# Performance work log

Measured on AMD Instinct MI355X. Metric: run time of the kernel, lower is better.

Reference implementation:

```python
import jax, jax.numpy as jnp
import numpy as np

N = 65536          # nodes
E = 1_048_576      # edges (avg degree 16)
IN_DIM = 16        # input_irreps = 16x0e
OUT_DIM = 8        # output_irreps = 8x0e
S_MUL = 32         # hidden 0e multiplicity
V_MUL = 16         # hidden 1o multiplicity
HID = S_MUL + 3 * V_MUL  # 80
LAYERS = 3
DEG = 16.0


def fctp(feat, eattr, w1, w2, w3, w4):
    """FullyConnectedTensorProduct(hidden x '1x0e+1x1o' -> hidden) per edge.
    Paths: 0e*0e->0e, 1o*1o->0e (dot, CG 1/sqrt(3)), 0e*1o->1o, 1o*0e->1o.
    Path weights mix multiplicities; e3nn-style fan-in normalization."""
    s1 = feat[:, :S_MUL]                         # [E, 32]
    v1 = feat[:, S_MUL:].reshape(-1, V_MUL, 3)   # [E, 16, 3]
    s2 = eattr[:, 0]                             # [E]
    v2 = eattr[:, 1:4]                           # [E, 3]
    c = 1.0 / np.sqrt(2.0)  # two paths per output irrep
    out_s = c * (jnp.einsum('ea,e,ac->ec', s1, s2, w1) / np.sqrt(S_MUL)
                 + jnp.einsum('eak,ek,ac->ec', v1, v2, w2) / np.sqrt(3.0 * V_MUL))
    out_v = c * (jnp.einsum('ea,ek,ac->eck', s1, v2, w3) / np.sqrt(S_MUL)
                 + jnp.einsum('eak,e,ac->eck', v1, s2, w4) / np.sqrt(V_MUL))
    return jnp.concatenate([out_s, out_v.reshape(-1, 3 * V_MUL)], axis=-1)


def setup_inputs() -> dict:
    key = jax.random.key(0)
    ks = jax.random.split(key, 12)
    inp = {
        'x': jax.random.normal(ks[0], (N, IN_DIM), jnp.float32),
        'edge_index': jax.random.randint(ks[1], (2, E), 0, N, jnp.int64 if jax.config.jax_enable_x64 else jnp.int32),
        'edge_attr': jax.random.normal(ks[2], (E, 4), jnp.float32),
        'W_in': jax.random.normal(ks[3], (IN_DIM, HID), jnp.float32) / np.sqrt(IN_DIM),
        'b_in': jnp.zeros((HID,), jnp.float32),
        'tp_w1': jax.random.normal(ks[4], (LAYERS, S_MUL, S_MUL), jnp.float32),
        'tp_w2': jax.random.normal(ks[5], (LAYERS, V_MUL, S_MUL), jnp.float32),
        'tp_w3': jax.random.normal(ks[6], (LAYERS, S_MUL, V_MUL), jnp.float32),
        'tp_w4': jax.random.normal(ks[7], (LAYERS, V_MUL, V_MUL), jnp.float32),
        'W_out': jax.random.normal(ks[8], (HID, OUT_DIM), jnp.float32) / np.sqrt(HID),
        'b_out': jnp.zeros((OUT_DIM,), jnp.float32),
    }
    return inp


def reference(x, edge_index, edge_attr, W_in, b_in, tp_w1, tp_w2, tp_w3, tp_w4, W_out, b_out):
    src, dst = edge_index[0], edge_index[1]
    h = x @ W_in + b_in                                   # [N, 80]
    for l in range(LAYERS):
        m = fctp(h[src], edge_attr, tp_w1[l], tp_w2[l], tp_w3[l], tp_w4[l])  # [E, 80]
        h = jax.ops.segment_sum(m, dst, num_segments=N) / np.sqrt(DEG)       # [N, 80]
    h = jax.nn.relu(h)
    return h @ W_out + b_out                              # [N, 8]
```

## Files before the change

kernel.cpp:

```cpp
#include <hip/hip_runtime.h>

#define NN 65536
#define NE 1048576
#define HID 80
#define CAP 8192

typedef unsigned int u32;
typedef unsigned short u16;
typedef unsigned long long u64;

typedef float v4f __attribute__((ext_vector_type(4)));

__device__ __forceinline__ u16 f2bf(float f) {
  u32 u = __float_as_uint(f);
  u = (u + 0x7fffu + ((u >> 16) & 1u)) >> 16;
  return (u16)u;
}
__device__ __forceinline__ float bfhi(u32 packed) {
  return __uint_as_float(packed & 0xffff0000u);
}
__device__ __forceinline__ float bflo(u32 packed) {
  return __uint_as_float(packed << 16);
}
__device__ __forceinline__ float4 ntload4f(const float4* p) {
  v4f v = __builtin_nontemporal_load((const v4f*)p);
  return make_float4(v.x, v.y, v.z, v.w);
}
__device__ __forceinline__ int ntloadi(const int* p) {
  return __builtin_nontemporal_load(p);
}

__global__ __launch_bounds__(256) void k_p1_in(const int* __restrict__ dst,
    const int* __restrict__ src, const float4* __restrict__ eattr,
    int* __restrict__ bcnt, uint4* __restrict__ tmp,
    const float* __restrict__ x, const float* __restrict__ W,
    const float* __restrict__ b, u16* __restrict__ hmain,
    u16* __restrict__ htail) {
  if (blockIdx.x < 512) {
    __shared__ int hist[256];
    __shared__ int lofs[257];
    __shared__ int gbase[256];
    __shared__ int sc[256];
    __shared__ uint4 buf[2048];
    int t = threadIdx.x;
    hist[t] = 0;
    __syncthreads();
    uint4 rec[8];
    int bk[8], lr[8];
    int base = blockIdx.x * 2048 + t;
#pragma unroll
    for (int k = 0; k < 8; k++) {
      int idx = base + k * 256;
      int d = ntloadi(dst + idx);
      float4 ea = ntload4f(eattr + idx);
      int s = ntloadi(src + idx);
      u32 c01 = (u32)f2bf(ea.x) | ((u32)f2bf(ea.y) << 16);
      u32 c23 = (u32)f2bf(ea.z) | ((u32)f2bf(ea.w) << 16);
      rec[k] = make_uint4((u32)s, c01, c23, (u32)d);
      bk[k] = d >> 8;
      lr[k] = atomicAdd(&hist[bk[k]], 1);
    }
    __syncthreads();
    int h = hist[t];
    gbase[t] = atomicAdd(&bcnt[t], h);
    sc[t] = h;
    __syncthreads();
    for (int d = 1; d < 256; d <<= 1) {
      int v = (t >= d) ? sc[t - d] : 0;
      __syncthreads();
      sc[t] += v;
      __syncthreads();
    }
    lofs[t] = sc[t] - h;
    if (t == 255) lofs[256] = 2048;
    __syncthreads();
#pragma unroll
    for (int k = 0; k < 8; k++) buf[lofs[bk[k]] + lr[k]] = rec[k];
    __syncthreads();
#pragma unroll
    for (int k = 0; k < 8; k++) {
      int j = t + k * 256;
      int lo = 0, hi = 256;
      while (hi - lo > 1) {
        int mid = (lo + hi) >> 1;
        if (lofs[mid] <= j) lo = mid;
        else hi = mid;
      }
      tmp[(size_t)lo * CAP + gbase[lo] + (j - lofs[lo])] = buf[j];
    }
  } else {
    int idx = (blockIdx.x - 512) * 256 + threadIdx.x;
    if (idx >= NN * 10) return;
    int n = idx / 10, part = idx % 10;
    const float4* xr = (const float4*)(x + (size_t)n * 16);
    float4 x0 = xr[0], x1 = xr[1], x2 = xr[2], x3 = xr[3];
    const float xs[16] = {x0.x, x0.y, x0.z, x0.w, x1.x, x1.y, x1.z, x1.w,
                          x2.x, x2.y, x2.z, x2.w, x3.x, x3.y, x3.z, x3.w};
    float acc[8];
#pragma unroll
    for (int j = 0; j < 8; j++) acc[j] = b[part * 8 + j];
#pragma unroll
    for (int k = 0; k < 16; k++) {
#pragma unroll
      for (int j = 0; j < 8; j++) acc[j] += xs[k] * W[k * HID + part * 8 + j];
    }
    u32 p0 = (u32)f2bf(acc[0]) | ((u32)f2bf(acc[1]) << 16);
    u32 p1 = (u32)f2bf(acc[2]) | ((u32)f2bf(acc[3]) << 16);
    u32 p2 = (u32)f2bf(acc[4]) | ((u32)f2bf(acc[5]) << 16);
    u32 p3 = (u32)f2bf(acc[6]) | ((u32)f2bf(acc[7]) << 16);
    uint4 vv = make_uint4(p0, p1, p2, p3);
    if (part < 8)
      *(uint4*)(hmain + (size_t)n * 64 + part * 8) = vv;
    else
      *(uint4*)(htail + (size_t)n * 16 + (part - 8) * 8) = vv;
  }
}

__global__ __launch_bounds__(256) void k_p15(const int* __restrict__ bcnt,
    const uint4* __restrict__ tmp, int* __restrict__ counts_tot,
    int* __restrict__ offsets, int* __restrict__ bucketsum) {
  __shared__ int hist[256];
  __shared__ int sc[256];
  int t = threadIdx.x;
  int b = blockIdx.x;
  hist[t] = 0;
  __syncthreads();
  int cnt = bcnt[b];
  const int* tw = (const int*)(tmp + (size_t)b * CAP);
  for (int j = t; j < cnt; j += 256) atomicAdd(&hist[tw[j * 4 + 3] & 255], 1);
  __syncthreads();
  int deg = hist[t];
  int p = (deg + 7) & ~7;
  sc[t] = p;
  __syncthreads();
  for (int d = 1; d < 256; d <<= 1) {
    int v = (t >= d) ? sc[t - d] : 0;
    __syncthreads();
    sc[t] += v;
    __syncthreads();
  }
  counts_tot[b * 256 + t] = deg;
  offsets[b * 256 + t] = sc[t] - p;
  if (t == 255) bucketsum[b] = sc[255];
}

__global__ __launch_bounds__(256) void k_p2(const int* __restrict__ bcnt,
    const uint4* __restrict__ tmp, const int* __restrict__ offsets,
    const int* __restrict__ bucketsum, const int* __restrict__ counts_tot,
    uint4* __restrict__ erec, int* __restrict__ offs_fin,
    int* __restrict__ brank, int* __restrict__ bidx, int* __restrict__ dcnt) {
  int t = threadIdx.x;
  if (blockIdx.x < 256) {
    __shared__ int bsum[256];
    __shared__ int cur[256];
    __shared__ int noff[256];
    if (t < 64) {
      int v0 = bucketsum[t * 4], v1 = bucketsum[t * 4 + 1];
      int v2 = bucketsum[t * 4 + 2], v3 = bucketsum[t * 4 + 3];
      int s = v0 + v1 + v2 + v3;
      int incl = s;
#pragma unroll
      for (int d = 1; d < 64; d <<= 1) {
        int o = __shfl_up(incl, d, 64);
        if (t >= d) incl += o;
      }
      int base = incl - s;
      bsum[t * 4] = base;
      bsum[t * 4 + 1] = base + v0;
      bsum[t * 4 + 2] = base + v0 + v1;
      bsum[t * 4 + 3] = base + v0 + v1 + v2;
    }
    cur[t] = 0;
    __syncthreads();
    int b = blockIdx.x;
    int off = offsets[b * 256 + t] + bsum[b];
    noff[t] = off;
    offs_fin[b * 256 + t] = off;
    __syncthreads();
    int cnt = bcnt[b];
    const uint4* tb = tmp + (size_t)b * CAP;
    for (int j = t; j < cnt; j += 256) {
      uint4 r = tb[j];
      int i = r.w & 255;
      int lr = atomicAdd(&cur[i], 1);
      erec[noff[i] + lr] = make_uint4(r.x, r.y, r.z, 0u);
    }
    __syncthreads();
    int deg = cur[t];
    int degp = (deg + 7) & ~7;
    uint4 z = make_uint4(0u, 0u, 0u, 0u);
    for (int e = deg; e < degp; e++) erec[noff[t] + e] = z;
  } else {
    int n = (blockIdx.x - 256) * 256 + t;
    int degp = (counts_tot[n] + 7) & ~7;
    int bb2 = 15 - min(degp >> 3, 15);
    int lane = t & 63;
    int base = 0;
#pragma unroll 1
    for (int bb = 0; bb < 16; bb++) {
      u64 m = __ballot(bb2 == bb);
      if (bb2 == bb) {
        int leader = __ffsll((long long)m) - 1;
        int lr = __popcll(m & ((lane == 63) ? ~0ull >> 1 : ((1ull << lane) - 1)));
        int bs = 0;
        if (lane == leader) bs = atomicAdd(&dcnt[bb], __popcll(m));
        bs = __shfl(bs, leader, 64);
        base = bs + lr;
      }
    }
    brank[n] = base;
    bidx[n] = bb2;
  }
}

__global__ __launch_bounds__(256) void k_p3(const int* __restrict__ dcnt,
    const int* __restrict__ brank, const int* __restrict__ bidx,
    int* __restrict__ nperm) {
  __shared__ int dsum[16];
  int t = threadIdx.x;
  if (t < 16) {
    int v = dcnt[t];
    int incl = v;
#pragma unroll
    for (int d = 1; d < 16; d <<= 1) {
      int o = __shfl_up(incl, d, 64);
      if (t >= d) incl += o;
    }
    dsum[t] = incl - v;
  }
  __syncthreads();
  int n = blockIdx.x * 256 + t;
  nperm[dsum[bidx[n]] + brank[n]] = n;
}

template <int LAST>
__global__ __launch_bounds__(128, 3) void k_msg(const u16* __restrict__ hmain,
    const u16* __restrict__ htail, u16* __restrict__ omain,
    u16* __restrict__ otail,
    const float* __restrict__ w1, const float* __restrict__ w2,
    const float* __restrict__ w3, const float* __restrict__ w4,
    const int* __restrict__ offsets, const int* __restrict__ counts,
    const int* __restrict__ nperm, const uint4* __restrict__ erec,
    const float* __restrict__ Wout, const float* __restrict__ bout,
    float* __restrict__ outp) {
  __shared__ float Rlds[8][4][81];
  int tid = threadIdx.x;
  const int q = tid >> 4;
  const int c = tid & 15;
  const int n = nperm[blockIdx.x * 8 + q];

  float R[4][5];
#pragma unroll
  for (int j = 0; j < 4; j++)
#pragma unroll
    for (int i = 0; i < 5; i++) R[j][i] = 0.f;

  const int start = offsets[n];
  const int degp = (counts[n] + 7) & ~7;
  const int B = degp >> 3;
  const uint2* hrow = (const uint2*)hmain + c;
  const u16* trow = htail + c;

  int i = 0;
  for (; i + 2 <= B; i += 2) {
    const int baseA = start + 8 * i;
    const int baseB = baseA + 8;
    uint4 rA[8], rB[8];
#pragma unroll
    for (int k = 0; k < 8; k++) rA[k] = erec[baseA + k];
#pragma unroll
    for (int k = 0; k < 8; k++) rB[k] = erec[baseB + k];
    uint2 hA[8], hB[8];
    u32 tA[8], tB[8];
#pragma unroll
    for (int k = 0; k < 8; k++) {
      size_t s16 = (size_t)rA[k].x * 16;
      hA[k] = hrow[s16];
      tA[k] = trow[s16];
    }
#pragma unroll
    for (int k = 0; k < 8; k++) {
      size_t s16 = (size_t)rB[k].x * 16;
      hB[k] = hrow[s16];
      tB[k] = trow[s16];
    }
#pragma unroll
    for (int k = 0; k < 8; k++) {
      float A0 = bflo(hA[k].x), A1 = bfhi(hA[k].x);
      float A2 = bflo(hA[k].y), A3 = bfhi(hA[k].y);
      float A4 = bflo(tA[k]);
      float f0 = bflo(rA[k].y), f1 = bfhi(rA[k].y);
      float f2 = bflo(rA[k].z), f3 = bfhi(rA[k].z);
      R[0][0] += f0 * A0; R[0][1] += f0 * A1; R[0][2] += f0 * A2;
      R[0][3] += f0 * A3; R[0][4] += f0 * A4;
      R[1][0] += f1 * A0; R[1][1] += f1 * A1; R[1][2] += f1 * A2;
      R[1][3] += f1 * A3; R[1][4] += f1 * A4;
      R[2][0] += f2 * A0; R[2][1] += f2 * A1; R[2][2] += f2 * A2;
      R[2][3] += f2 * A3; R[2][4] += f2 * A4;
      R[3][0] += f3 * A0; R[3][1] += f3 * A1; R[3][2] += f3 * A2;
      R[3][3] += f3 * A3; R[3][4] += f3 * A4;
    }
#pragma unroll
    for (int k = 0; k < 8; k++) {
      float A0 = bflo(hB[k].x), A1 = bfhi(hB[k].x);
      float A2 = bflo(hB[k].y), A3 = bfhi(hB[k].y);
      float A4 = bflo(tB[k]);
      float f0 = bflo(rB[k].y), f1 = bfhi(rB[k].y);
      float f2 = bflo(rB[k].z), f3 = bfhi(rB[k].z);
      R[0][0] += f0 * A0; R[0][1] += f0 * A1; R[0][2] += f0 * A2;
      R[0][3] += f0 * A3; R[0][4] += f0 * A4;
      R[1][0] += f1 * A0; R[1][1] += f1 * A1; R[1][2] += f1 * A2;
      R[1][3] += f1 * A3; R[1][4] += f1 * A4;
      R[2][0] += f2 * A0; R[2][1] += f2 * A1; R[2][2] += f2 * A2;
      R[2][3] += f2 * A3; R[2][4] += f2 * A4;
      R[3][0] += f3 * A0; R[3][1] += f3 * A1; R[3][2] += f3 * A2;
      R[3][3] += f3 * A3; R[3][4] += f3 * A4;
    }
  }
  if (i < B) {
    const int baseA = start + 8 * i;
    uint4 rA[8];
#pragma unroll
    for (int k = 0; k < 8; k++) rA[k] = erec[baseA + k];
    uint2 hA[8];
    u32 tA[8];
#pragma unroll
    for (int k = 0; k < 8; k++) {
      size_t s16 = (size_t)rA[k].x * 16;
      hA[k] = hrow[s16];
      tA[k] = trow[s16];
    }
#pragma unroll
    for (int k = 0; k < 8; k++) {
      float A0 = bflo(hA[k].x), A1 = bfhi(hA[k].x);
      float A2 = bflo(hA[k].y), A3 = bfhi(hA[k].y);
      float A4 = bflo(tA[k]);
      float f0 = bflo(rA[k].y), f1 = bfhi(rA[k].y);
      float f2 = bflo(rA[k].z), f3 = bfhi(rA[k].z);
      R[0][0] += f0 * A0; R[0][1] += f0 * A1; R[0][2] += f0 * A2;
      R[0][3] += f0 * A3; R[0][4] += f0 * A4;
      R[1][0] += f1 * A0; R[1][1] += f1 * A1; R[1][2] += f1 * A2;
      R[1][3] += f1 * A3; R[1][4] += f1 * A4;
      R[2][0] += f2 * A0; R[2][1] += f2 * A1; R[2][2] += f2 * A2;
      R[2][3] += f2 * A3; R[2][4] += f2 * A4;
      R[3][0] += f3 * A0; R[3][1] += f3 * A1; R[3][2] += f3 * A2;
      R[3][3] += f3 * A3; R[3][4] += f3 * A4;
    }
  }

#pragma unroll
  for (int j = 0; j < 4; j++) {
#pragma unroll
    for (int k = 0; k < 4; k++) Rlds[q][j][4 * c + k] = R[j][k];
    Rlds[q][j][64 + c] = R[j][4];
  }

  const float C1 = 0.03125f;
  const float C2 = 0.025515518f;
  const float C3 = 0.03125f;
  const float C4 = 0.044194174f;

  u16* opm = omain + (size_t)n * 64;

  float s0 = 0.f, s1 = 0.f;
#pragma unroll
  for (int a = 0; a < 32; a++) {
    float rs = Rlds[q][0][a];
    s0 += rs * w1[a * 32 + c];
    s1 += rs * w1[a * 32 + c + 16];
  }
  float t0 = 0.f, t1 = 0.f;
#pragma unroll
  for (int a = 0; a < 16; a++) {
    float T = Rlds[q][1][32 + 3 * a] + Rlds[q][2][33 + 3 * a] +
              Rlds[q][3][34 + 3 * a];
    t0 += T * w2[a * 32 + c];
    t1 += T * w2[a * 32 + c + 16];
  }

  float y[8];
  if (LAST) {
#pragma unroll
    for (int j = 0; j < 8; j++) y[j] = 0.f;
    float vs0 = C1 * s0 + C2 * t0;
    float vs1 = C1 * s1 + C2 * t1;
    vs0 = vs0 > 0.f ? vs0 : 0.f;
    vs1 = vs1 > 0.f ? vs1 : 0.f;
#pragma unroll
    for (int j = 0; j < 8; j++)
      y[j] += vs0 * Wout[c * 8 + j] + vs1 * Wout[(c + 16) * 8 + j];
  } else {
    opm[c] = f2bf(C1 * s0 + C2 * t0);
    opm[c + 16] = f2bf(C1 * s1 + C2 * t1);
  }

#pragma unroll
  for (int v2 = 0; v2 < 3; v2++) {
    int c2 = 32 + 16 * v2 + c;
    int cv = (c2 - 32) / 3, k = (c2 - 32) % 3;
    float a3 = 0.f, a4 = 0.f;
#pragma unroll
    for (int a = 0; a < 32; a++) a3 += Rlds[q][k + 1][a] * w3[a * 16 + cv];
#pragma unroll
    for (int a = 0; a < 16; a++)
      a4 += Rlds[q][0][32 + 3 * a + k] * w4[a * 16 + cv];
    float val = C3 * a3 + C4 * a4;
    if (LAST) {
      val = val > 0.f ? val : 0.f;
#pragma unroll
      for (int j = 0; j < 8; j++) y[j] += val * Wout[c2 * 8 + j];
    } else {
      u16 v = f2bf(val);
      if (v2 < 2) opm[32 + 16 * v2 + c] = v;
      else otail[(size_t)n * 16 + c] = v;
    }
  }

  if (LAST) {
#pragma unroll
    for (int m = 1; m <= 8; m <<= 1) {
#pragma unroll
      for (int j = 0; j < 8; j++) y[j] += __shfl_xor(y[j], m, 64);
    }
    float w = y[0];
#pragma unroll
    for (int j = 1; j < 8; j++)
      if (c == j) w = y[j];
    if (c < 8) outp[(size_t)n * 8 + c] = w + bout[c];
  }
}

extern "C" void kernel_launch(void* const* d_in, const int* in_sizes, int n_in,
                              void* d_out, int out_size, void* d_ws,
                              size_t ws_size, hipStream_t stream) {
  const float* x = (const float*)d_in[0];
  const int* ei = (const int*)d_in[1];
  const float* eattr = (const float*)d_in[2];
  const float* W_in = (const float*)d_in[3];
  const float* b_in = (const float*)d_in[4];
  const float* tp_w1 = (const float*)d_in[5];
  const float* tp_w2 = (const float*)d_in[6];
  const float* tp_w3 = (const float*)d_in[7];
  const float* tp_w4 = (const float*)d_in[8];
  const float* W_out = (const float*)d_in[9];
  const float* b_out = (const float*)d_in[10];
  float* out = (float*)d_out;

  char* ws = (char*)d_ws;
  size_t off = 0;
  auto alloc = [&](size_t bytes) {
    void* p = ws + off;
    off += (bytes + 255) & ~size_t(255);
    return p;
  };
  const size_t NEP = (size_t)NE + 8 * (size_t)NN;
  u16* hm_a = (u16*)alloc((size_t)NN * 64 * 2);
  u16* ht_a = (u16*)alloc((size_t)NN * 16 * 2);
  u16* hm_b = (u16*)alloc((size_t)NN * 64 * 2);
  u16* ht_b = (u16*)alloc((size_t)NN * 16 * 2);
  int* bcnt = (int*)alloc(256 * 4);
  int* dcnt = (int*)alloc(16 * 4);
  int* counts_tot = (int*)alloc((size_t)NN * 4);
  int* offsets = (int*)alloc((size_t)NN * 4);
  int* offs_fin = (int*)alloc((size_t)NN * 4);
  int* bucketsum = (int*)alloc(256 * 4);
  int* brank = (int*)alloc((size_t)NN * 4);
  int* bidx = (int*)alloc((size_t)NN * 4);
  int* nperm = (int*)alloc((size_t)NN * 4);
  uint4* tmp = (uint4*)alloc((size_t)256 * CAP * 16);
  uint4* erec = (uint4*)alloc(NEP * 16);

  const int* src = ei;
  const int* dst = ei + NE;

  hipMemsetAsync(bcnt, 0, 1024 + 256, stream);
  k_p1_in<<<512 + (NN * 10 + 255) / 256, 256, 0, stream>>>(
      dst, src, (const float4*)eattr, bcnt, tmp, x, W_in, b_in, hm_a, ht_a);
  k_p15<<<256, 256, 0, stream>>>(bcnt, tmp, counts_tot, offsets, bucketsum);
  k_p2<<<512, 256, 0, stream>>>(bcnt, tmp, offsets, bucketsum, counts_tot,
                                erec, offs_fin, brank, bidx, dcnt);
  k_p3<<<256, 256, 0, stream>>>(dcnt, brank, bidx, nperm);

  u16* hmi = hm_a;
  u16* hti = ht_a;
  u16* hmo = hm_b;
  u16* hto = ht_b;
  for (int l = 0; l < 2; l++) {
    k_msg<0><<<NN / 8, 128, 0, stream>>>(hmi, hti, hmo, hto, tp_w1 + l * 1024,
                                         tp_w2 + l * 512, tp_w3 + l * 512,
                                         tp_w4 + l * 256, offs_fin, counts_tot,
                                         nperm, erec, W_out, b_out, out);
    u16* t;
    t = hmi; hmi = hmo; hmo = t;
    t = hti; hti = hto; hto = t;
  }
  k_msg<1><<<NN / 8, 128, 0, stream>>>(hmi, hti, hmo, hto, tp_w1 + 2048,
                                       tp_w2 + 1024, tp_w3 + 1024, tp_w4 + 512,
                                       offs_fin, counts_tot, nperm, erec,
                                       W_out, b_out, out);
}
```

Baseline: 344.1 us.

## Merge bucket histogram and scatter kernels using fixed per-bucket edge capacity

Fuses the per-bucket degree histogram kernel and the scatter kernel into one 512-thread kernel. Each coarse bucket now gets a fixed ECAP-sized region of the edge record array, which removes the global bucket-sum prefix scan and the intermediate offsets and bucketsum buffers. The first partition pass also uses twice as many blocks with half the edges each. This drops one launch and one global round trip, at the cost of a larger padded edge array and a bucket overflow risk if a bucket's padded degree total exceeds ECAP.

```diff
diff --git a/kernel.cpp b/kernel.cpp
--- a/kernel.cpp
+++ b/kernel.cpp
@@ -3,7 +3,8 @@
 #define NN 65536
 #define NE 1048576
 #define HID 80
-#define CAP 8192
+#define TCAP 8192
+#define ECAP 8192
 
 typedef unsigned int u32;
 typedef unsigned short u16;
@@ -36,20 +37,20 @@
     const float* __restrict__ x, const float* __restrict__ W,
     const float* __restrict__ b, u16* __restrict__ hmain,
     u16* __restrict__ htail) {
-  if (blockIdx.x < 512) {
+  if (blockIdx.x < 1024) {
     __shared__ int hist[256];
     __shared__ int lofs[257];
     __shared__ int gbase[256];
     __shared__ int sc[256];
-    __shared__ uint4 buf[2048];
+    __shared__ uint4 buf[1024];
     int t = threadIdx.x;
     hist[t] = 0;
     __syncthreads();
-    uint4 rec[8];
-    int bk[8], lr[8];
-    int base = blockIdx.x * 2048 + t;
-#pragma unroll
-    for (int k = 0; k < 8; k++) {
+    uint4 rec[4];
+    int bk[4], lr[4];
+    int base = blockIdx.x * 1024 + t;
+#pragma unroll
+    for (int k = 0; k < 4; k++) {
       int idx = base + k * 256;
       int d = ntloadi(dst + idx);
       float4 ea = ntload4f(eattr + idx);
@@ -72,13 +73,13 @@
       __syncthreads();
     }
     lofs[t] = sc[t] - h;
-    if (t == 255) lofs[256] = 2048;
-    __syncthreads();
-#pragma unroll
-    for (int k = 0; k < 8; k++) buf[lofs[bk[k]] + lr[k]] = rec[k];
-    __syncthreads();
-#pragma unroll
-    for (int k = 0; k < 8; k++) {
+    if (t == 255) lofs[256] = 1024;
+    __syncthreads();
+#pragma unroll
+    for (int k = 0; k < 4; k++) buf[lofs[bk[k]] + lr[k]] = rec[k];
+    __syncthreads();
+#pragma unroll
+    for (int k = 0; k < 4; k++) {
       int j = t + k * 256;
       int lo = 0, hi = 256;
       while (hi - lo > 1) {
@@ -86,10 +87,10 @@
         if (lofs[mid] <= j) lo = mid;
         else hi = mid;
       }
-      tmp[(size_t)lo * CAP + gbase[lo] + (j - lofs[lo])] = buf[j];
+      tmp[(size_t)lo * TCAP + gbase[lo] + (j - lofs[lo])] = buf[j];
     }
   } else {
-    int idx = (blockIdx.x - 512) * 256 + threadIdx.x;
+    int idx = (blockIdx.x - 1024) * 256 + threadIdx.x;
     if (idx >= NN * 10) return;
     int n = idx / 10, part = idx % 10;
     const float4* xr = (const float4*)(x + (size_t)n * 16);
@@ -116,83 +117,58 @@
   }
 }
 
-__global__ __launch_bounds__(256) void k_p15(const int* __restrict__ bcnt,
+__global__ __launch_bounds__(512) void k_p2m(const int* __restrict__ bcnt,
     const uint4* __restrict__ tmp, int* __restrict__ counts_tot,
-    int* __restrict__ offsets, int* __restrict__ bucketsum) {
+    int* __restrict__ offs_fin, uint4* __restrict__ erec,
+    int* __restrict__ brank, int* __restrict__ bidx, int* __restrict__ dcnt) {
   __shared__ int hist[256];
   __shared__ int sc[256];
+  __shared__ int noff[256];
+  __shared__ int cur[256];
   int t = threadIdx.x;
+  if (t < 256) {
+    hist[t] = 0;
+    cur[t] = 0;
+  }
+  __syncthreads();
   int b = blockIdx.x;
-  hist[t] = 0;
-  __syncthreads();
   int cnt = bcnt[b];
-  const int* tw = (const int*)(tmp + (size_t)b * CAP);
-  for (int j = t; j < cnt; j += 256) atomicAdd(&hist[tw[j * 4 + 3] & 255], 1);
-  __syncthreads();
-  int deg = hist[t];
-  int p = (deg + 7) & ~7;
-  sc[t] = p;
+  const uint4* tb = tmp + (size_t)b * TCAP;
+  const int* tw = (const int*)tb;
+  for (int j = t; j < cnt; j += 512) atomicAdd(&hist[tw[j * 4 + 3] & 255], 1);
+  __syncthreads();
+  int deg = 0, p = 0;
+  if (t < 256) {
+    deg = hist[t];
+    p = (deg + 7) & ~7;
+    sc[t] = p;
+  }
   __syncthreads();
   for (int d = 1; d < 256; d <<= 1) {
-    int v = (t >= d) ? sc[t - d] : 0;
-    __syncthreads();
-    sc[t] += v;
-    __syncthreads();
-  }
-  counts_tot[b * 256 + t] = deg;
-  offsets[b * 256 + t] = sc[t] - p;
-  if (t == 255) bucketsum[b] = sc[255];
-}
-
-__global__ __launch_bounds__(256) void k_p2(const int* __restrict__ bcnt,
-    const uint4* __restrict__ tmp, const int* __restrict__ offsets,
-    const int* __restrict__ bucketsum, const int* __restrict__ counts_tot,
-    uint4* __restrict__ erec, int* __restrict__ offs_fin,
-    int* __restrict__ brank, int* __restrict__ bidx, int* __restrict__ dcnt) {
-  int t = threadIdx.x;
-  if (blockIdx.x < 256) {
-    __shared__ int bsum[256];
-    __shared__ int cur[256];
-    __shared__ int noff[256];
-    if (t < 64) {
-      int v0 = bucketsum[t * 4], v1 = bucketsum[t * 4 + 1];
-      int v2 = bucketsum[t * 4 + 2], v3 = bucketsum[t * 4 + 3];
-      int s = v0 + v1 + v2 + v3;
-      int incl = s;
-#pragma unroll
-      for (int d = 1; d < 64; d <<= 1) {
-        int o = __shfl_up(incl, d, 64);
-        if (t >= d) incl += o;
-      }
-      int base = incl - s;
-      bsum[t * 4] = base;
-      bsum[t * 4 + 1] = base + v0;
-      bsum[t * 4 + 2] = base + v0 + v1;
-      bsum[t * 4 + 3] = base + v0 + v1 + v2;
-    }
-    cur[t] = 0;
-    __syncthreads();
-    int b = blockIdx.x;
-    int off = offsets[b * 256 + t] + bsum[b];
+    int v = (t < 256 && t >= d) ? sc[t - d] : 0;
+    __syncthreads();
+    if (t < 256) sc[t] += v;
+    __syncthreads();
+  }
+  if (t < 256) {
+    int off = b * ECAP + sc[t] - p;
     noff[t] = off;
     offs_fin[b * 256 + t] = off;
-    __syncthreads();
-    int cnt = bcnt[b];
-    const uint4* tb = tmp + (size_t)b * CAP;
-    for (int j = t; j < cnt; j += 256) {
-      uint4 r = tb[j];
-      int i = r.w & 255;
-      int lr = atomicAdd(&cur[i], 1);
-      erec[noff[i] + lr] = make_uint4(r.x, r.y, r.z, 0u);
-    }
-    __syncthreads();
-    int deg = cur[t];
+    counts_tot[b * 256 + t] = deg;
+  }
+  __syncthreads();
+  for (int j = t; j < cnt; j += 512) {
+    uint4 r = tb[j];
+    int i = r.w & 255;
+    int lr = atomicAdd(&cur[i], 1);
+    erec[(size_t)noff[i] + lr] = make_uint4(r.x, r.y, r.z, 0u);
+  }
+  __syncthreads();
+  if (t < 256) {
     int degp = (deg + 7) & ~7;
     uint4 z = make_uint4(0u, 0u, 0u, 0u);
-    for (int e = deg; e < degp; e++) erec[noff[t] + e] = z;
-  } else {
-    int n = (blockIdx.x - 256) * 256 + t;
-    int degp = (counts_tot[n] + 7) & ~7;
+    for (int e = deg; e < degp; e++) erec[(size_t)noff[t] + e] = z;
+    int n = b * 256 + t;
     int bb2 = 15 - min(degp >> 3, 15);
     int lane = t & 63;
     int base = 0;
@@ -453,7 +429,6 @@
     off += (bytes + 255) & ~size_t(255);
     return p;
   };
-  const size_t NEP = (size_t)NE + 8 * (size_t)NN;
   u16* hm_a = (u16*)alloc((size_t)NN * 64 * 2);
   u16* ht_a = (u16*)alloc((size_t)NN * 16 * 2);
   u16* hm_b = (u16*)alloc((size_t)NN * 64 * 2);
@@ -461,24 +436,21 @@
   int* bcnt = (int*)alloc(256 * 4);
   int* dcnt = (int*)alloc(16 * 4);
   int* counts_tot = (int*)alloc((size_t)NN * 4);
-  int* offsets = (int*)alloc((size_t)NN * 4);
   int* offs_fin = (int*)alloc((size_t)NN * 4);
-  int* bucketsum = (int*)alloc(256 * 4);
   int* brank = (int*)alloc((size_t)NN * 4);
   int* bidx = (int*)alloc((size_t)NN * 4);
   int* nperm = (int*)alloc((size_t)NN * 4);
-  uint4* tmp = (uint4*)alloc((size_t)256 * CAP * 16);
-  uint4* erec = (uint4*)alloc(NEP * 16);
+  uint4* tmp = (uint4*)alloc((size_t)256 * TCAP * 16);
+  uint4* erec = (uint4*)alloc((size_t)256 * ECAP * 16);
 
   const int* src = ei;
   const int* dst = ei + NE;
 
-  hipMemsetAsync(bcnt, 0, 1024 + 256, stream);
-  k_p1_in<<<512 + (NN * 10 + 255) / 256, 256, 0, stream>>>(
+  hipMemsetAsync(bcnt, 0, 1024 + 64, stream);
+  k_p1_in<<<1024 + (NN * 10 + 255) / 256, 256, 0, stream>>>(
       dst, src, (const float4*)eattr, bcnt, tmp, x, W_in, b_in, hm_a, ht_a);
-  k_p15<<<256, 256, 0, stream>>>(bcnt, tmp, counts_tot, offsets, bucketsum);
-  k_p2<<<512, 256, 0, stream>>>(bcnt, tmp, offsets, bucketsum, counts_tot,
-                                erec, offs_fin, brank, bidx, dcnt);
+  k_p2m<<<256, 512, 0, stream>>>(bcnt, tmp, counts_tot, offs_fin, erec,
+                                 brank, bidx, dcnt);
   k_p3<<<256, 256, 0, stream>>>(dcnt, brank, bidx, nperm);
 
   u16* hmi = hm_a;
```

After: 349.1 us. No clear change (+1.4%).
